# Kernel optimization log

Measured on AMD Instinct MI355X. Metric: run time of the kernel, lower is better.

The kernel has to match this reference:

```python
import jax, jax.numpy as jnp
import numpy as np
from jax import lax

UNIT = 0.11  # pairing threshold from sort_w(weight, 0.11)


def _greedy_pairs(wflat, unit=UNIT):
    """Faithful greedy pairing from sort_w: for each out-channel dd, scan flat
    indices a ascending; pair a with the first unoccupied b>a with
    |w[a]+w[b]|<=unit. Returns gather indices src and signs such that
    Weff[dd,i] = sign[dd,i] * Wflat[dd, src[dd,i]] reproduces vicsum_v2."""
    d, m = wflat.shape
    src = np.tile(np.arange(m, dtype=np.int32), (d, 1))
    sign = np.ones((d, m), dtype=np.float32)
    for dd in range(d):
        occ = np.zeros(m, dtype=bool)
        row = wflat[dd]
        for a in range(m - 1):
            if occ[a]:
                continue
            cand = np.nonzero((~occ[a + 1:]) & (np.abs(row[a] + row[a + 1:]) <= unit))[0]
            if cand.size:
                b = a + 1 + int(cand[0])
                occ[a] = occ[b] = True
                src[dd, b] = a     # out += (x[a]-x[b])*w[a]  =>  coeff at b is -w[a]
                sign[dd, b] = -1.0
    return src, sign


def _make_conv(rng, d, c, k):
    bound = 1.0 / np.sqrt(c * k * k)  # torch default uniform init scale
    w = rng.uniform(-bound, bound, size=(d, c, k, k)).astype(np.float32)
    b = rng.uniform(-bound, bound, size=(d,)).astype(np.float32)
    src, sign = _greedy_pairs(w.reshape(d, -1))
    return w, b, src, sign


def setup_inputs() -> dict:
    rng = np.random.default_rng(0)
    x = rng.standard_normal((16384, 1, 32, 32)).astype(np.float32)
    w1, b1, src1, sign1 = _make_conv(rng, 6, 1, 5)
    w2, b2, src2, sign2 = _make_conv(rng, 16, 6, 5)
    w3, b3, src3, sign3 = _make_conv(rng, 120, 16, 5)
    bf1 = 1.0 / np.sqrt(120.0)
    fc1_w = rng.uniform(-bf1, bf1, size=(84, 120)).astype(np.float32)
    fc1_b = rng.uniform(-bf1, bf1, size=(84,)).astype(np.float32)
    bf2 = 1.0 / np.sqrt(84.0)
    fc2_w = rng.uniform(-bf2, bf2, size=(10, 84)).astype(np.float32)
    fc2_b = rng.uniform(-bf2, bf2, size=(10,)).astype(np.float32)
    return {
        'x': jnp.asarray(x),
        'w1': jnp.asarray(w1), 'b1': jnp.asarray(b1), 'sign1': jnp.asarray(sign1),
        'w2': jnp.asarray(w2), 'b2': jnp.asarray(b2), 'sign2': jnp.asarray(sign2),
        'w3': jnp.asarray(w3), 'b3': jnp.asarray(b3), 'sign3': jnp.asarray(sign3),
        'fc1_w': jnp.asarray(fc1_w), 'fc1_b': jnp.asarray(fc1_b),
        'fc2_w': jnp.asarray(fc2_w), 'fc2_b': jnp.asarray(fc2_b),
        'src1': jnp.asarray(src1), 'src2': jnp.asarray(src2), 'src3': jnp.asarray(src3),
        'TRIGGERed': 1, 'count': 0,
    }


def _eff_weight(w, src, sign):
    d = w.shape[0]
    wflat = w.reshape(d, -1)
    weff = jnp.take_along_axis(wflat, src, axis=1) * sign
    return weff.reshape(w.shape)


def _conv(x, w, b):
    y = lax.conv_general_dilated(x, w, window_strides=(1, 1), padding='VALID',
                                 dimension_numbers=('NCHW', 'OIHW', 'NCHW'))
    return y + b[None, :, None, None]


def _avgpool2(x):
    n, c, h, w = x.shape
    return x.reshape(n, c, h // 2, 2, w // 2, 2).mean(axis=(3, 5))


def reference(x, w1, b1, sign1, w2, b2, sign2, w3, b3, sign3,
              fc1_w, fc1_b, fc2_w, fc2_b, src1, src2, src3, TRIGGERed, count):
    if TRIGGERed:
        h = _avgpool2(jax.nn.sigmoid(_conv(x, _eff_weight(w1, src1, sign1), b1)))
        h = _avgpool2(jax.nn.sigmoid(_conv(h, _eff_weight(w2, src2, sign2), b2)))
        h = jax.nn.sigmoid(_conv(h, _eff_weight(w3, src3, sign3), b3))
    else:
        h = _avgpool2(jax.nn.sigmoid(_conv(x, w1, b1)))
        h = _avgpool2(jax.nn.sigmoid(_conv(h, w2, b2)))
        h = jax.nn.sigmoid(_conv(h, w3, b3))
    h = h.reshape(h.shape[0], -1)                     # [N, 120]
    h = jax.nn.sigmoid(h @ fc1_w.T + fc1_b)           # [N, 84]
    return h @ fc2_w.T + fc2_b                        # [N, 10]
```

## Files before the change

### kernel.cpp

```cpp
#include <hip/hip_runtime.h>

#define THREADS 256

__device__ __forceinline__ float sigmoidf(float x) {
    return __builtin_amdgcn_rcpf(1.0f + __expf(-x));
}

#define E2OFF 168
#define E3OFF 2856
#define P1OFF 54056

__global__ void weff_prep(const float* __restrict__ w1, const float* __restrict__ sg1, const int* __restrict__ sr1,
                          const float* __restrict__ w2, const float* __restrict__ sg2, const int* __restrict__ sr2,
                          const float* __restrict__ w3, const float* __restrict__ sg3, const int* __restrict__ sr3,
                          const int* __restrict__ trig, float* __restrict__ ws) {
    int i = blockIdx.x * blockDim.x + threadIdx.x;
    const int t = trig[0];
    if (i < 168) {
        int c = i / 28, k = i % 28;
        float v = 0.f;
        if (k < 25) { int f = c * 25 + k; v = t ? sg1[f] * w1[c * 25 + sr1[f]] : w1[f]; }
        ws[i] = v;
    } else if (i < E3OFF) {
        int j = i - E2OFF;
        int oc = j / 168, r = j % 168, ic = r / 28, k = r % 28;
        float v = 0.f;
        if (k < 25) { int f = oc * 150 + ic * 25 + k; v = t ? sg2[f] * w2[oc * 150 + sr2[f]] : w2[f]; }
        ws[i] = v;
    } else if (i < P1OFF) {
        int idx = i - E3OFF;
        int j  = idx & 3;
        int l  = (idx >> 2) & 63;
        int kw = idx >> 8;
        int k  = kw % 50, wt = kw / 50;
        int c  = (wt << 5) | (l >> 1);
        int h  = l & 1;
        float v = 0.f;
        if (c < 120) {
            int e = c * 400 + h * 200 + k * 4 + j;
            v = t ? sg3[e] * w3[c * 400 + sr3[e]] : w3[e];
        }
        ws[i] = v;
    }
}

__global__ __launch_bounds__(THREADS, 4)
void k_conv1(const float* __restrict__ x, const float* __restrict__ ws,
             const float* __restrict__ b1, float* __restrict__ p1, int nimg) {
    __shared__ __align__(16) float lw[176];
    const int tid = threadIdx.x;
    if (tid < 168) lw[tid] = ws[tid];
    if (tid >= 168 && tid < 174) lw[tid] = b1[tid - 168];
    __syncthreads();

    int g = blockIdx.x * THREADS + tid;
    if (g >= nimg * 98) return;
    const int img = g / 98, rem = g % 98;
    const int r = rem / 7, t = rem % 7;

    const float* xb = x + (size_t)img * 1024 + (2 * r) * 32 + 4 * t;
    float pt[6][8];
    #pragma unroll
    for (int rr = 0; rr < 6; ++rr) {
        const float4 v0 = *reinterpret_cast<const float4*>(xb + rr * 32);
        const float4 v1 = *reinterpret_cast<const float4*>(xb + rr * 32 + 4);
        pt[rr][0] = v0.x; pt[rr][1] = v0.y; pt[rr][2] = v0.z; pt[rr][3] = v0.w;
        pt[rr][4] = v1.x; pt[rr][5] = v1.y; pt[rr][6] = v1.z; pt[rr][7] = v1.w;
    }

    #pragma unroll
    for (int c = 0; c < 6; ++c) {
        float z[2][4];
        #pragma unroll
        for (int p = 0; p < 2; ++p)
            #pragma unroll
            for (int w = 0; w < 4; ++w) z[p][w] = 0.f;

        #pragma unroll
        for (int k4 = 0; k4 < 6; ++k4) {
            const float4 w4 = *reinterpret_cast<const float4*>(&lw[c * 28 + 4 * k4]);
            #pragma unroll
            for (int j = 0; j < 4; ++j) {
                const int k = 4 * k4 + j;
                const int ky = k / 5, kx = k % 5;
                const float wv = (j == 0) ? w4.x : (j == 1) ? w4.y : (j == 2) ? w4.z : w4.w;
                #pragma unroll
                for (int p = 0; p < 2; ++p)
                    #pragma unroll
                    for (int dy = 0; dy < 2; ++dy)
                        #pragma unroll
                        for (int dx = 0; dx < 2; ++dx)
                            z[p][2 * dy + dx] += pt[dy + ky][2 * p + dx + kx] * wv;
            }
        }
        {
            const float wv = lw[c * 28 + 24];
            #pragma unroll
            for (int p = 0; p < 2; ++p)
                #pragma unroll
                for (int dy = 0; dy < 2; ++dy)
                    #pragma unroll
                    for (int dx = 0; dx < 2; ++dx)
                        z[p][2 * dy + dx] += pt[dy + 4][2 * p + dx + 4] * wv;
        }

        const float bb = lw[168 + c];
        const float s0 = sigmoidf(z[0][0] + bb) + sigmoidf(z[0][1] + bb) +
                         sigmoidf(z[0][2] + bb) + sigmoidf(z[0][3] + bb);
        const float s1 = sigmoidf(z[1][0] + bb) + sigmoidf(z[1][1] + bb) +
                         sigmoidf(z[1][2] + bb) + sigmoidf(z[1][3] + bb);
        *reinterpret_cast<float2*>(&p1[((size_t)img * 6 + c) * 196 + r * 14 + 2 * t]) =
            make_float2(0.25f * s0, 0.25f * s1);
    }
}

__global__ __launch_bounds__(THREADS, 3)
void k_conv2(const float* __restrict__ p1, const float* __restrict__ ws,
             const float* __restrict__ b2, float* __restrict__ p2, int nimg) {
    int g = blockIdx.x * THREADS + threadIdx.x;
    if (g >= nimg * 25) return;
    const int img = g / 25, pix = g % 25;
    const int pi = pix / 5, pj = pix % 5;
    const float* pimg = p1 + (size_t)img * 1176 + (2 * pi) * 14 + 2 * pj;
    const float* wq = ws + E2OFF;

    #pragma unroll 1
    for (int half = 0; half < 2; ++half) {
        float acc[8][4];
        #pragma unroll
        for (int oc = 0; oc < 8; ++oc)
            #pragma unroll
            for (int w = 0; w < 4; ++w) acc[oc][w] = 0.f;

        for (int ic = 0; ic < 6; ++ic) {
            float pt[6][6];
            const float* pb = pimg + ic * 196;
            #pragma unroll
            for (int r = 0; r < 6; ++r) {
                #pragma unroll
                for (int cc = 0; cc < 3; ++cc) {
                    float2 v = *reinterpret_cast<const float2*>(pb + r * 14 + 2 * cc);
                    pt[r][2 * cc] = v.x; pt[r][2 * cc + 1] = v.y;
                }
            }
            const int wbase = half * 1344 + ic * 28;
            #pragma unroll
            for (int oc = 0; oc < 8; ++oc) {
                const float* wr = wq + wbase + oc * 168;
                #pragma unroll
                for (int k4 = 0; k4 < 6; ++k4) {
                    const float4 w4 = *reinterpret_cast<const float4*>(wr + 4 * k4);
                    #pragma unroll
                    for (int j = 0; j < 4; ++j) {
                        const int k = 4 * k4 + j;
                        const int ky = k / 5, kx = k % 5;
                        const float wv = (j == 0) ? w4.x : (j == 1) ? w4.y : (j == 2) ? w4.z : w4.w;
                        acc[oc][0] += pt[ky][kx] * wv;
                        acc[oc][1] += pt[ky][kx + 1] * wv;
                        acc[oc][2] += pt[ky + 1][kx] * wv;
                        acc[oc][3] += pt[ky + 1][kx + 1] * wv;
                    }
                }
                const float wv = wr[24];
                acc[oc][0] += pt[4][4] * wv; acc[oc][1] += pt[4][5] * wv;
                acc[oc][2] += pt[5][4] * wv; acc[oc][3] += pt[5][5] * wv;
            }
        }

        #pragma unroll
        for (int oc = 0; oc < 8; ++oc) {
            const int c = half * 8 + oc;
            const float bb = b2[c];
            const float s = sigmoidf(acc[oc][0] + bb) + sigmoidf(acc[oc][1] + bb) +
                            sigmoidf(acc[oc][2] + bb) + sigmoidf(acc[oc][3] + bb);
            p2[(size_t)img * 400 + c * 25 + pix] = 0.25f * s;
        }
    }
}

#define K3_IMG 8
__global__ __launch_bounds__(THREADS, 4)
void k_tail(const float* __restrict__ p2, const float* __restrict__ ws,
            const float* __restrict__ b3,
            const float* __restrict__ fc1w, const float* __restrict__ fc1b,
            const float* __restrict__ fc2w, const float* __restrict__ fc2b,
            float* __restrict__ out, int nimg) {
    __shared__ __align__(16) float sp2[K3_IMG][400];
    __shared__ __align__(16) float v3[K3_IMG][120];
    __shared__ __align__(16) float v4[K3_IMG][84];
    const int tid = threadIdx.x;
    const int img0 = blockIdx.x * K3_IMG;

    for (int i = tid; i < K3_IMG * 100; i += THREADS) {
        const int im = i / 100, off = i % 100;
        const int gi = min(img0 + im, nimg - 1);
        reinterpret_cast<float4*>(&sp2[im][0])[off] =
            reinterpret_cast<const float4*>(p2 + (size_t)gi * 400)[off];
    }
    __syncthreads();

    if (tid < 240) {
        const int h = tid & 1;
        const int wt = tid >> 6, l = tid & 63;
        const float4* wp = reinterpret_cast<const float4*>(ws + E3OFF);
        float4 a[K3_IMG];
        #pragma unroll
        for (int im = 0; im < K3_IMG; ++im) a[im] = make_float4(0.f, 0.f, 0.f, 0.f);
        #pragma unroll 5
        for (int k = 0; k < 50; ++k) {
            const float4 w4 = wp[(wt * 50 + k) * 64 + l];
            #pragma unroll
            for (int im = 0; im < K3_IMG; ++im) {
                const float4 u = *reinterpret_cast<const float4*>(&sp2[im][h * 200 + 4 * k]);
                a[im].x += u.x * w4.x; a[im].y += u.y * w4.y;
                a[im].z += u.z * w4.z; a[im].w += u.w * w4.w;
            }
        }
        const int c = tid >> 1;
        #pragma unroll
        for (int im = 0; im < K3_IMG; ++im) {
            float z = (a[im].x + a[im].y) + (a[im].z + a[im].w);
            z += __shfl_xor(z, 1, 64);
            if (h == 0) v3[im][c] = sigmoidf(z + b3[c]);
        }
    }
    __syncthreads();

    for (int it = tid; it < K3_IMG * 84; it += THREADS) {
        const int im = it / 84, j = it % 84;
        const float4* wp = reinterpret_cast<const float4*>(fc1w + j * 120);
        const float4* vp = reinterpret_cast<const float4*>(&v3[im][0]);
        float4 a = make_float4(0.f, 0.f, 0.f, 0.f);
        #pragma unroll 6
        for (int k = 0; k < 30; ++k) {
            const float4 w4 = wp[k];
            const float4 u = vp[k];
            a.x += u.x * w4.x; a.y += u.y * w4.y;
            a.z += u.z * w4.z; a.w += u.w * w4.w;
        }
        v4[im][j] = sigmoidf((a.x + a.y) + (a.z + a.w) + fc1b[j]);
    }
    __syncthreads();

    if (tid < K3_IMG * 10) {
        const int im = tid / 10, j = tid % 10;
        if (img0 + im < nimg) {
            const float4* wp = reinterpret_cast<const float4*>(fc2w + j * 84);
            const float4* vp = reinterpret_cast<const float4*>(&v4[im][0]);
            float4 a = make_float4(0.f, 0.f, 0.f, 0.f);
            #pragma unroll
            for (int k = 0; k < 21; ++k) {
                const float4 w4 = wp[k];
                const float4 u = vp[k];
                a.x += u.x * w4.x; a.y += u.y * w4.y;
                a.z += u.z * w4.z; a.w += u.w * w4.w;
            }
            out[(size_t)(img0 + im) * 10 + j] = (a.x + a.y) + (a.z + a.w) + fc2b[j];
        }
    }
}

__device__ __forceinline__ float wget_ig(const float* __restrict__ wp,
                                         const float* __restrict__ sg,
                                         const int* __restrict__ sr,
                                         int row, int m, int idx, bool tg) {
    int f = row * m + idx;
    return tg ? sg[f] * wp[row * m + sr[f]] : wp[f];
}

__global__ __launch_bounds__(THREADS, 4)
void lenet_fused(const float* __restrict__ x,
                 const float* __restrict__ w1e, const float* __restrict__ b1,
                 const float* __restrict__ w2e, const float* __restrict__ b2,
                 const float* __restrict__ w3e, const float* __restrict__ b3,
                 const float* __restrict__ fc1w, const float* __restrict__ fc1b,
                 const float* __restrict__ fc2w, const float* __restrict__ fc2b,
                 const float* __restrict__ sg1, const int* __restrict__ sr1,
                 const float* __restrict__ sg2, const int* __restrict__ sr2,
                 const float* __restrict__ sg3, const int* __restrict__ sr3,
                 const int* __restrict__ trig,
                 float* __restrict__ out, int nimg) {
    const int tid = threadIdx.x;
    const int img0 = blockIdx.x * 2;
    __shared__ __align__(16) float xs[2][1024];
    __shared__ __align__(16) float p1[2][6][196];
    __shared__ __align__(16) float p2[2][400];
    __shared__ __align__(16) float v3[2][120];
    __shared__ __align__(16) float v4[2][84];
    const bool tg = trig[0] != 0;

    #pragma unroll
    for (int im = 0; im < 2; ++im) {
        int gi = min(img0 + im, nimg - 1);
        reinterpret_cast<float4*>(&xs[im][0])[tid] =
            reinterpret_cast<const float4*>(x + (size_t)gi * 1024)[tid];
    }
    __syncthreads();

    for (int it = tid; it < 2 * 196; it += THREADS) {
        const int img = it / 196, pix = it % 196;
        const int pi = pix / 14, pj = pix % 14;
        const float* xb = &xs[img][(2 * pi) * 32 + 2 * pj];
        float pt[6][6];
        #pragma unroll
        for (int r = 0; r < 6; ++r)
            #pragma unroll
            for (int cc = 0; cc < 3; ++cc) {
                float2 v = *reinterpret_cast<const float2*>(&xb[r * 32 + cc * 2]);
                pt[r][cc * 2] = v.x; pt[r][cc * 2 + 1] = v.y;
            }
        #pragma unroll
        for (int c = 0; c < 6; ++c) {
            float z0 = 0.f, z1 = 0.f, z2 = 0.f, z3 = 0.f;
            #pragma unroll
            for (int ky = 0; ky < 5; ++ky)
                #pragma unroll
                for (int kx = 0; kx < 5; ++kx) {
                    const float wv = wget_ig(w1e, sg1, sr1, c, 25, ky * 5 + kx, tg);
                    z0 += pt[ky][kx] * wv;     z1 += pt[ky][kx + 1] * wv;
                    z2 += pt[ky + 1][kx] * wv; z3 += pt[ky + 1][kx + 1] * wv;
                }
            const float bb = b1[c];
            p1[img][c][pix] = 0.25f * (sigmoidf(z0 + bb) + sigmoidf(z1 + bb) +
                                       sigmoidf(z2 + bb) + sigmoidf(z3 + bb));
        }
    }
    __syncthreads();

    if (tid < 200) {
        const int img = tid / 100, rem = tid % 100;
        const int pix = rem >> 2, win = rem & 3;
        const int di = win >> 1, dj = win & 1;
        const int pi = pix / 5, pj = pix % 5;
        const int r0 = 2 * pi + di, c0 = 2 * pj + dj;
        float acc[16];
        #pragma unroll
        for (int c = 0; c < 16; ++c) acc[c] = 0.f;
        for (int ic = 0; ic < 6; ++ic) {
            float pt[5][5];
            #pragma unroll
            for (int ky = 0; ky < 5; ++ky)
                #pragma unroll
                for (int kx = 0; kx < 5; ++kx)
                    pt[ky][kx] = p1[img][ic][(r0 + ky) * 14 + (c0 + kx)];
            #pragma unroll
            for (int c = 0; c < 16; ++c) {
                float z = acc[c];
                #pragma unroll
                for (int ky = 0; ky < 5; ++ky)
                    #pragma unroll
                    for (int kx = 0; kx < 5; ++kx)
                        z += pt[ky][kx] * wget_ig(w2e, sg2, sr2, c, 150, ic * 25 + ky * 5 + kx, tg);
                acc[c] = z;
            }
        }
        #pragma unroll
        for (int c = 0; c < 16; ++c) {
            float z = sigmoidf(acc[c] + b2[c]);
            z += __shfl_xor(z, 1, 64);
            z += __shfl_xor(z, 2, 64);
            if (win == 0) p2[img][c * 25 + pix] = 0.25f * z;
        }
    }
    __syncthreads();

    if (tid < 240) {
        const int c = tid >> 1, h = tid & 1;
        float s0 = 0.f, s1 = 0.f;
        for (int k = 0; k < 200; ++k) {
            float wv = wget_ig(w3e, sg3, sr3, c, 400, h * 200 + k, tg);
            s0 += p2[0][h * 200 + k] * wv;
            s1 += p2[1][h * 200 + k] * wv;
        }
        s0 += __shfl_xor(s0, 1, 64);
        s1 += __shfl_xor(s1, 1, 64);
        if (h == 0) {
            const float bb = b3[c];
            v3[0][c] = sigmoidf(s0 + bb);
            v3[1][c] = sigmoidf(s1 + bb);
        }
    }
    __syncthreads();

    if (tid < 168) {
        const int img = tid / 84, j = tid % 84;
        float a = 0.f;
        for (int k = 0; k < 120; ++k) a += v3[img][k] * fc1w[j * 120 + k];
        v4[img][j] = sigmoidf(a + fc1b[j]);
    }
    __syncthreads();

    if (tid < 20) {
        const int img = tid / 10, j = tid % 10;
        if (img0 + img < nimg) {
            float a = 0.f;
            for (int k = 0; k < 84; ++k) a += v4[img][k] * fc2w[j * 84 + k];
            out[(size_t)(img0 + img) * 10 + j] = a + fc2b[j];
        }
    }
}

extern "C" void kernel_launch(void* const* d_in, const int* in_sizes, int n_in,
                              void* d_out, int out_size, void* d_ws, size_t ws_size,
                              hipStream_t stream) {
    const float* x    = (const float*)d_in[0];
    const float* w1   = (const float*)d_in[1];
    const float* b1   = (const float*)d_in[2];
    const float* sg1  = (const float*)d_in[3];
    const float* w2   = (const float*)d_in[4];
    const float* b2   = (const float*)d_in[5];
    const float* sg2  = (const float*)d_in[6];
    const float* w3   = (const float*)d_in[7];
    const float* b3   = (const float*)d_in[8];
    const float* sg3  = (const float*)d_in[9];
    const float* fc1w = (const float*)d_in[10];
    const float* fc1b = (const float*)d_in[11];
    const float* fc2w = (const float*)d_in[12];
    const float* fc2b = (const float*)d_in[13];
    const int*   sr1  = (const int*)d_in[14];
    const int*   sr2  = (const int*)d_in[15];
    const int*   sr3  = (const int*)d_in[16];
    const int*   trig = (const int*)d_in[17];

    const int nimg = in_sizes[0] / 1024;
    float* out = (float*)d_out;

    const size_t p1off = P1OFF;
    const size_t p2off = p1off + (size_t)nimg * 1176;
    const size_t need_bytes = (p2off + (size_t)nimg * 400) * sizeof(float);

    if (ws_size >= need_bytes) {
        float* ws = (float*)d_ws;
        weff_prep<<<(P1OFF + 255) / 256, 256, 0, stream>>>(
            w1, sg1, sr1, w2, sg2, sr2, w3, sg3, sr3, trig, ws);
        k_conv1<<<(nimg * 98 + THREADS - 1) / THREADS, THREADS, 0, stream>>>(
            x, ws, b1, ws + p1off, nimg);
        k_conv2<<<(nimg * 25 + THREADS - 1) / THREADS, THREADS, 0, stream>>>(
            ws + p1off, ws, b2, ws + p2off, nimg);
        k_tail<<<(nimg + K3_IMG - 1) / K3_IMG, THREADS, 0, stream>>>(
            ws + p2off, ws, b3, fc1w, fc1b, fc2w, fc2b, out, nimg);
    } else {
        lenet_fused<<<(nimg + 1) / 2, THREADS, 0, stream>>>(
            x, w1, b1, w2, b2, w3, b3,
            fc1w, fc1b, fc2w, fc2b, sg1, sr1, sg2, sr2, sg3, sr3, trig, out, nimg);
    }
}
```

Before: 232.7 us.

## Restructure conv3 tail: one thread per channel with broadcast p2 reads

Repacks the conv3 effective weights into a [k][128 channels] float4 layout so each thread owns one output channel and walks all 100 float4 taps. The tail kernel drops 128 threads per block, no longer stages p2 in shared memory, and reads each image's p2 row straight from global memory as a wavefront-uniform broadcast. This removes the LDS staging, the sync and the lane-pair shuffle reduction. In exchange it relies on cache hits for the repeated uniform global loads and runs a longer serial dot product per thread.

Measured after the change: 254.1 us. 9.2% more time.

```diff
diff --git a/kernel.cpp b/kernel.cpp
--- a/kernel.cpp
+++ b/kernel.cpp
@@ -30,14 +30,12 @@
     } else if (i < P1OFF) {
         int idx = i - E3OFF;
         int j  = idx & 3;
-        int l  = (idx >> 2) & 63;
-        int kw = idx >> 8;
-        int k  = kw % 50, wt = kw / 50;
-        int c  = (wt << 5) | (l >> 1);
-        int h  = l & 1;
+        int f4 = idx >> 2;
+        int c  = f4 & 127;
+        int k  = f4 >> 7;
         float v = 0.f;
         if (c < 120) {
-            int e = c * 400 + h * 200 + k * 4 + j;
+            int e = c * 400 + k * 4 + j;
             v = t ? sg3[e] * w3[c * 400 + sr3[e]] : w3[e];
         }
         ws[i] = v;
@@ -178,62 +176,51 @@
     }
 }
 
-#define K3_IMG 8
-__global__ __launch_bounds__(THREADS, 4)
+#define T2_IMG 8
+__global__ __launch_bounds__(128, 8)
 void k_tail(const float* __restrict__ p2, const float* __restrict__ ws,
             const float* __restrict__ b3,
             const float* __restrict__ fc1w, const float* __restrict__ fc1b,
             const float* __restrict__ fc2w, const float* __restrict__ fc2b,
             float* __restrict__ out, int nimg) {
-    __shared__ __align__(16) float sp2[K3_IMG][400];
-    __shared__ __align__(16) float v3[K3_IMG][120];
-    __shared__ __align__(16) float v4[K3_IMG][84];
+    __shared__ __align__(16) float v3[T2_IMG][120];
+    __shared__ __align__(16) float v4[T2_IMG][84];
     const int tid = threadIdx.x;
-    const int img0 = blockIdx.x * K3_IMG;
-
-    for (int i = tid; i < K3_IMG * 100; i += THREADS) {
-        const int im = i / 100, off = i % 100;
-        const int gi = min(img0 + im, nimg - 1);
-        reinterpret_cast<float4*>(&sp2[im][0])[off] =
-            reinterpret_cast<const float4*>(p2 + (size_t)gi * 400)[off];
-    }
-    __syncthreads();
-
-    if (tid < 240) {
-        const int h = tid & 1;
-        const int wt = tid >> 6, l = tid & 63;
-        const float4* wp = reinterpret_cast<const float4*>(ws + E3OFF);
-        float4 a[K3_IMG];
-        #pragma unroll
-        for (int im = 0; im < K3_IMG; ++im) a[im] = make_float4(0.f, 0.f, 0.f, 0.f);
-        #pragma unroll 5
-        for (int k = 0; k < 50; ++k) {
-            const float4 w4 = wp[(wt * 50 + k) * 64 + l];
-            #pragma unroll
-            for (int im = 0; im < K3_IMG; ++im) {
-                const float4 u = *reinterpret_cast<const float4*>(&sp2[im][h * 200 + 4 * k]);
-                a[im].x += u.x * w4.x; a[im].y += u.y * w4.y;
-                a[im].z += u.z * w4.z; a[im].w += u.w * w4.w;
-            }
-        }
-        const int c = tid >> 1;
-        #pragma unroll
-        for (int im = 0; im < K3_IMG; ++im) {
-            float z = (a[im].x + a[im].y) + (a[im].z + a[im].w);
-            z += __shfl_xor(z, 1, 64);
-            if (h == 0) v3[im][c] = sigmoidf(z + b3[c]);
-        }
-    }
-    __syncthreads();
-
-    for (int it = tid; it < K3_IMG * 84; it += THREADS) {
+    const int img0 = blockIdx.x * T2_IMG;
+
+    float acc[T2_IMG];
+    #pragma unroll
+    for (int im = 0; im < T2_IMG; ++im) acc[im] = 0.f;
+
+    const float4* wp = reinterpret_cast<const float4*>(ws + E3OFF);
+    #pragma unroll 2
+    for (int k = 0; k < 100; ++k) {
+        const float4 w4 = wp[k * 128 + tid];
+        #pragma unroll
+        for (int im = 0; im < T2_IMG; ++im) {
+            const int gi = min(img0 + im, nimg - 1);
+            const float4 u = *reinterpret_cast<const float4*>(
+                p2 + (size_t)gi * 400 + 4 * k);
+            acc[im] += w4.x * u.x + w4.y * u.y + w4.z * u.z + w4.w * u.w;
+        }
+    }
+
+    if (tid < 120) {
+        const float bb = b3[tid];
+        #pragma unroll
+        for (int im = 0; im < T2_IMG; ++im)
+            v3[im][tid] = sigmoidf(acc[im] + bb);
+    }
+    __syncthreads();
+
+    for (int it = tid; it < T2_IMG * 84; it += 128) {
         const int im = it / 84, j = it % 84;
-        const float4* wp = reinterpret_cast<const float4*>(fc1w + j * 120);
+        const float4* wp1 = reinterpret_cast<const float4*>(fc1w + j * 120);
         const float4* vp = reinterpret_cast<const float4*>(&v3[im][0]);
         float4 a = make_float4(0.f, 0.f, 0.f, 0.f);
         #pragma unroll 6
         for (int k = 0; k < 30; ++k) {
-            const float4 w4 = wp[k];
+            const float4 w4 = wp1[k];
             const float4 u = vp[k];
             a.x += u.x * w4.x; a.y += u.y * w4.y;
             a.z += u.z * w4.z; a.w += u.w * w4.w;
@@ -242,15 +229,15 @@
     }
     __syncthreads();
 
-    if (tid < K3_IMG * 10) {
+    if (tid < T2_IMG * 10) {
         const int im = tid / 10, j = tid % 10;
         if (img0 + im < nimg) {
-            const float4* wp = reinterpret_cast<const float4*>(fc2w + j * 84);
+            const float4* wp2 = reinterpret_cast<const float4*>(fc2w + j * 84);
             const float4* vp = reinterpret_cast<const float4*>(&v4[im][0]);
             float4 a = make_float4(0.f, 0.f, 0.f, 0.f);
             #pragma unroll
             for (int k = 0; k < 21; ++k) {
-                const float4 w4 = wp[k];
+                const float4 w4 = wp2[k];
                 const float4 u = vp[k];
                 a.x += u.x * w4.x; a.y += u.y * w4.y;
                 a.z += u.z * w4.z; a.w += u.w * w4.w;
@@ -437,7 +424,7 @@
             x, ws, b1, ws + p1off, nimg);
         k_conv2<<<(nimg * 25 + THREADS - 1) / THREADS, THREADS, 0, stream>>>(
             ws + p1off, ws, b2, ws + p2off, nimg);
-        k_tail<<<(nimg + K3_IMG - 1) / K3_IMG, THREADS, 0, stream>>>(
+        k_tail<<<(nimg + T2_IMG - 1) / T2_IMG, 128, 0, stream>>>(
             ws + p2off, ws, b3, fc1w, fc1b, fc2w, fc2b, out, nimg);
     } else {
         lenet_fused<<<(nimg + 1) / 2, THREADS, 0, stream>>>(
```
